# Kernel tuning notes

Hardware: AMD Instinct MI355X
Metric: run time of the kernel (lower is better)

Reference implementation:

```python
import jax, jax.numpy as jnp
import numpy as np

B, L, D_MODEL = 2, 2048, 1024
D_INNER, D_STATE, D_CONV, DT_RANK = 2048, 16, 4, 64  # expand=2, dt_rank=ceil(1024/16)


def setup_inputs() -> dict:
    key = jax.random.key(0)
    ks = jax.random.split(key, 12)
    s = lambda k, shape, sc=0.02: jax.random.normal(k, shape, dtype=jnp.float32) * sc
    return {
        "x": jax.random.normal(ks[0], (B, L, D_MODEL), dtype=jnp.float32),
        "norm_w": jnp.ones((D_MODEL,), jnp.float32),
        "norm_b": jnp.zeros((D_MODEL,), jnp.float32),
        "in_proj_w": s(ks[1], (2 * D_INNER, D_MODEL)),
        "conv_w": s(ks[2], (D_INNER, 1, D_CONV), 0.1),
        "conv_b": s(ks[3], (D_INNER,), 0.1),
        "x_proj_w": s(ks[4], (DT_RANK + 2 * D_STATE, D_INNER)),
        "dt_proj_w": s(ks[5], (D_INNER, DT_RANK), 0.1),
        "dt_proj_b": s(ks[6], (D_INNER,), 0.5),
        "A_log": jnp.log(jnp.broadcast_to(jnp.arange(1, D_STATE + 1, dtype=jnp.float32), (D_INNER, D_STATE))),
        "D": jnp.ones((D_INNER,), jnp.float32),
        "out_proj_w": s(ks[7], (D_MODEL, D_INNER)),
    }


def _layernorm(x, w, b, eps=1e-5):
    mu = jnp.mean(x, axis=-1, keepdims=True)
    var = jnp.var(x, axis=-1, keepdims=True)
    return (x - mu) * jax.lax.rsqrt(var + eps) * w + b


def _mamba_forward(x, norm_w, norm_b, in_proj_w, conv_w, conv_b, x_proj_w,
                   dt_proj_w, dt_proj_b, A_log, D, out_proj_w):
    residual = x
    xn = _layernorm(x, norm_w, norm_b)
    # in_proj -> split into x-branch and gate z
    xz = jnp.einsum('bld,ed->ble', xn, in_proj_w)  # [B,L,2*D_INNER]
    xc, z = jnp.split(xz, 2, axis=-1)
    # causal depthwise conv1d over time
    xt = jnp.transpose(xc, (0, 2, 1))  # [B,C,L]
    xt = jnp.pad(xt, ((0, 0), (0, 0), (D_CONV - 1, 0)))
    xt = jax.lax.conv_general_dilated(
        xt, conv_w, window_strides=(1,), padding=[(0, 0)],
        feature_group_count=D_INNER,
        dimension_numbers=('NCH', 'OIH', 'NCH')) + conv_b[None, :, None]
    u = jax.nn.silu(jnp.transpose(xt, (0, 2, 1)))  # [B,L,D_INNER]
    # input-dependent dt, B, C
    x_dbl = jnp.einsum('bld,ed->ble', u, x_proj_w)
    dt, Bm, Cm = jnp.split(x_dbl, [DT_RANK, DT_RANK + D_STATE], axis=-1)
    dt = jax.nn.softplus(jnp.einsum('blr,dr->bld', dt, dt_proj_w) + dt_proj_b)  # [B,L,D_INNER]
    A = -jnp.exp(A_log)  # [D_INNER, D_STATE]

    def step(h, inp):
        dt_t, B_t, C_t, u_t = inp  # [B,Di],[B,Ds],[B,Ds],[B,Di]
        dA = jnp.exp(dt_t[..., None] * A)                       # [B,Di,Ds]
        h = dA * h + (dt_t * u_t)[..., None] * B_t[:, None, :]  # [B,Di,Ds]
        y_t = jnp.einsum('bds,bs->bd', h, C_t)
        return h, y_t

    xs = (jnp.transpose(dt, (1, 0, 2)), jnp.transpose(Bm, (1, 0, 2)),
          jnp.transpose(Cm, (1, 0, 2)), jnp.transpose(u, (1, 0, 2)))
    h0 = jnp.zeros((B, D_INNER, D_STATE), dtype=x.dtype)
    _, ys = jax.lax.scan(step, h0, xs)
    y = jnp.transpose(ys, (1, 0, 2)) + u * D  # [B,L,D_INNER]
    y = y * jax.nn.silu(z)
    out = jnp.einsum('ble,de->bld', y, out_proj_w)
    # dropout in eval mode = identity
    return residual + out


def reference(x, norm_w, norm_b, in_proj_w, conv_w, conv_b, x_proj_w,
              dt_proj_w, dt_proj_b, A_log, D, out_proj_w):
    return _mamba_forward(x, norm_w, norm_b, in_proj_w, conv_w, conv_b, x_proj_w,
                          dt_proj_w, dt_proj_b, A_log, D, out_proj_w)
```

## Files before the change

### kernel.cpp

```cpp
#include <hip/hip_runtime.h>
#include <hip/hip_bf16.h>
#include <math.h>

#define BB 2
#define LL 2048
#define DMODEL 1024
#define DINNER 2048
#define DSTATE 16
#define DTRANK 64
#define NROWS (BB * LL)
#define NC 64
#define CK 32
#define KS 16
#define KCH (DINNER / KS)

typedef __bf16 bf16x8 __attribute__((ext_vector_type(8)));
typedef float  f32x4  __attribute__((ext_vector_type(4)));
typedef ushort us8    __attribute__((ext_vector_type(8)));
typedef __attribute__((address_space(3))) void       as3_void;
typedef const __attribute__((address_space(1))) void as1_cvoid;

__device__ __forceinline__ ushort f2bf(float x) {
    __hip_bfloat16 h = __float2bfloat16(x);
    return *(ushort*)&h;
}
__device__ __forceinline__ float bf2f(ushort u) {
    unsigned int v = ((unsigned int)u) << 16;
    return *(float*)&v;
}

__global__ __launch_bounds__(256) void ln_kernel(const float* __restrict__ x,
                                                 const float* __restrict__ w,
                                                 const float* __restrict__ b,
                                                 __hip_bfloat16* __restrict__ xn) {
    int row = blockIdx.x;
    const float* xr = x + (size_t)row * DMODEL;
    float4 v = reinterpret_cast<const float4*>(xr)[threadIdx.x];
    float s  = v.x + v.y + v.z + v.w;
    float ss = v.x * v.x + v.y * v.y + v.z * v.z + v.w * v.w;
    for (int off = 32; off > 0; off >>= 1) {
        s  += __shfl_down(s, off);
        ss += __shfl_down(ss, off);
    }
    __shared__ float red0[4], red1[4];
    __shared__ float mu_s, rstd_s;
    int lane = threadIdx.x & 63, wv = threadIdx.x >> 6;
    if (lane == 0) { red0[wv] = s; red1[wv] = ss; }
    __syncthreads();
    if (threadIdx.x == 0) {
        float S = red0[0] + red0[1] + red0[2] + red0[3];
        float SS = red1[0] + red1[1] + red1[2] + red1[3];
        float mu = S * (1.0f / DMODEL);
        float var = SS * (1.0f / DMODEL) - mu * mu;
        mu_s = mu;
        rstd_s = rsqrtf(var + 1e-5f);
    }
    __syncthreads();
    float mu = mu_s, rstd = rstd_s;
    float4 wv4 = reinterpret_cast<const float4*>(w)[threadIdx.x];
    float4 bv4 = reinterpret_cast<const float4*>(b)[threadIdx.x];
    ushort4 o;
    o.x = f2bf((v.x - mu) * rstd * wv4.x + bv4.x);
    o.y = f2bf((v.y - mu) * rstd * wv4.y + bv4.y);
    o.z = f2bf((v.z - mu) * rstd * wv4.z + bv4.z);
    o.w = f2bf((v.w - mu) * rstd * wv4.w + bv4.w);
    *reinterpret_cast<ushort4*>((ushort*)xn + (size_t)row * DMODEL + threadIdx.x * 4) = o;
}

__global__ __launch_bounds__(256) void cvt_kernel(const float* __restrict__ in,
                                                  __hip_bfloat16* __restrict__ o) {
    int i = (blockIdx.x * 256 + threadIdx.x) * 4;
    float4 v = *reinterpret_cast<const float4*>(in + i);
    ushort4 p;
    p.x = f2bf(v.x); p.y = f2bf(v.y); p.z = f2bf(v.z); p.w = f2bf(v.w);
    *reinterpret_cast<ushort4*>((ushort*)o + i) = p;
}

template <int EPI>
__global__ __launch_bounds__(256) void gemm_bf16(
    const __hip_bfloat16* __restrict__ A, int lda,
    const __hip_bfloat16* __restrict__ W, int ldw,
    void* __restrict__ C, void* __restrict__ C2, int nsplit, int ldc,
    int K, const float* __restrict__ R) {
    __shared__ ushort As[128][32];
    __shared__ ushort Bs[128][32];
    int tid = threadIdx.x;
    int w = tid >> 6, lane = tid & 63;
    int m0 = blockIdx.y * 128, n0 = blockIdx.x * 128;
    int wr = w >> 1, wc = w & 1;

    int srow = (w << 4) + (lane >> 2);
    int skoff = (lane & 3) << 3;
    const ushort* gA = (const ushort*)A + (size_t)(m0 + srow) * lda + skoff;
    const ushort* gB = (const ushort*)W + (size_t)(n0 + srow) * ldw + skoff;
    char* ldsA0 = (char*)&As[0][0] + w * 1024;
    char* ldsB0 = (char*)&Bs[0][0] + w * 1024;

    f32x4 acc[4][4] = {};
    int frow = (lane & 15);
    int fk   = (lane >> 4) << 3;

    for (int k0 = 0; k0 < K; k0 += 32) {
        __syncthreads();
        __builtin_amdgcn_global_load_lds((as1_cvoid*)(gA + k0),                    (as3_void*)(ldsA0),        16, 0, 0);
        __builtin_amdgcn_global_load_lds((as1_cvoid*)(gA + (size_t)64 * lda + k0), (as3_void*)(ldsA0 + 4096), 16, 0, 0);
        __builtin_amdgcn_global_load_lds((as1_cvoid*)(gB + k0),                    (as3_void*)(ldsB0),        16, 0, 0);
        __builtin_amdgcn_global_load_lds((as1_cvoid*)(gB + (size_t)64 * ldw + k0), (as3_void*)(ldsB0 + 4096), 16, 0, 0);
        __syncthreads();

        bf16x8 af[4], bfr[4];
#pragma unroll
        for (int mi = 0; mi < 4; mi++)
            af[mi] = *(const bf16x8*)&As[wr * 64 + mi * 16 + frow][fk];
#pragma unroll
        for (int ni = 0; ni < 4; ni++)
            bfr[ni] = *(const bf16x8*)&Bs[wc * 64 + ni * 16 + frow][fk];
#pragma unroll
        for (int mi = 0; mi < 4; mi++)
#pragma unroll
            for (int ni = 0; ni < 4; ni++)
                acc[mi][ni] = __builtin_amdgcn_mfma_f32_16x16x32_bf16(
                    af[mi], bfr[ni], acc[mi][ni], 0, 0, 0);
    }

    int crow = (lane >> 4) << 2;
    int ccol = lane & 15;
    bool toz = (EPI == 0) && (n0 >= nsplit);
    int nbase = toz ? (n0 - nsplit) : n0;
    ushort* Cu = toz ? (ushort*)C2 : (ushort*)C;
#pragma unroll
    for (int mi = 0; mi < 4; mi++) {
#pragma unroll
        for (int ni = 0; ni < 4; ni++) {
#pragma unroll
            for (int r = 0; r < 4; r++) {
                int m = m0 + wr * 64 + mi * 16 + crow + r;
                int n = nbase + wc * 64 + ni * 16 + ccol;
                float v = acc[mi][ni][r];
                if (EPI == 2) {
                    v += R[(size_t)m * ldc + n];
                    ((float*)C)[(size_t)m * ldc + n] = v;
                } else if (EPI == 1) {
                    v += R[n];
                    v = (v > 20.f) ? v : log1pf(__expf(v));
                    ((ushort*)C)[(size_t)m * ldc + n] = f2bf(v);
                } else {
                    Cu[(size_t)m * ldc + n] = f2bf(v);
                }
            }
        }
    }
}

__global__ __launch_bounds__(256) void xp_partial(
    const ushort* __restrict__ A,
    const float* __restrict__ W,
    float* __restrict__ P) {
    __shared__ float As[16][64];
    __shared__ float Ws[16][64];
    int m0 = blockIdx.y * 64;
    int n0 = blockIdx.x * 64;
    int kbase = blockIdx.z * KCH;
    int tid = threadIdx.x;
    int tm = tid >> 4, tn = tid & 15;
    int lr = tid >> 2;
    int lk = (tid & 3) << 2;

    float acc[4][4] = {};

    for (int k0 = kbase; k0 < kbase + KCH; k0 += 16) {
        ushort4 au = *reinterpret_cast<const ushort4*>(A + (size_t)(m0 + lr) * DINNER + k0 + lk);
        float4 av = make_float4(bf2f(au.x), bf2f(au.y), bf2f(au.z), bf2f(au.w));
        float4 wvv;
        int wn = n0 + lr;
        if (wn < 96)
            wvv = *reinterpret_cast<const float4*>(W + (size_t)wn * DINNER + k0 + lk);
        else
            wvv = make_float4(0.f, 0.f, 0.f, 0.f);
        __syncthreads();
        As[lk + 0][lr] = av.x; As[lk + 1][lr] = av.y;
        As[lk + 2][lr] = av.z; As[lk + 3][lr] = av.w;
        Ws[lk + 0][lr] = wvv.x; Ws[lk + 1][lr] = wvv.y;
        Ws[lk + 2][lr] = wvv.z; Ws[lk + 3][lr] = wvv.w;
        __syncthreads();
#pragma unroll
        for (int k = 0; k < 16; k++) {
            float4 a = *reinterpret_cast<const float4*>(&As[k][tm << 2]);
            float4 bv = *reinterpret_cast<const float4*>(&Ws[k][tn << 2]);
            float ar[4] = {a.x, a.y, a.z, a.w};
            float br[4] = {bv.x, bv.y, bv.z, bv.w};
#pragma unroll
            for (int i = 0; i < 4; i++)
#pragma unroll
                for (int j = 0; j < 4; j++)
                    acc[i][j] = fmaf(ar[i], br[j], acc[i][j]);
        }
    }
    float* Pz = P + (size_t)blockIdx.z * NROWS * 96;
#pragma unroll
    for (int i = 0; i < 4; i++) {
        int m = m0 + (tm << 2) + i;
#pragma unroll
        for (int j = 0; j < 4; j++) {
            int n = n0 + (tn << 2) + j;
            if (n < 96)
                Pz[(size_t)m * 96 + n] = acc[i][j];
        }
    }
}

__global__ __launch_bounds__(256) void xp_reduce(
    const float* __restrict__ P, float* __restrict__ xdbl,
    ushort* __restrict__ xdbl16) {
    int i = blockIdx.x * 256 + threadIdx.x;
    float s = 0.f;
#pragma unroll
    for (int z = 0; z < KS; z++)
        s += P[(size_t)z * NROWS * 96 + i];
    xdbl[i] = s;
    xdbl16[i] = f2bf(s);
}

__global__ __launch_bounds__(256) void conv_silu_kernel(
    const ushort* __restrict__ xc16, const float* __restrict__ cw,
    const float* __restrict__ cb, ushort* __restrict__ u16) {
    int r = blockIdx.x;
    int l = r & (LL - 1);
    int c0 = threadIdx.x << 3;
    const ushort* base = xc16 + (size_t)r * DINNER + c0;
    us8 z8 = {0, 0, 0, 0, 0, 0, 0, 0};
    us8 v0 = *(const us8*)(base);
    us8 v1 = (l >= 1) ? *(const us8*)(base - DINNER)     : z8;
    us8 v2 = (l >= 2) ? *(const us8*)(base - 2 * DINNER) : z8;
    us8 v3 = (l >= 3) ? *(const us8*)(base - 3 * DINNER) : z8;
    us8 o;
#pragma unroll
    for (int j = 0; j < 8; j++) {
        float4 wj = reinterpret_cast<const float4*>(cw)[c0 + j];
        float acc = cb[c0 + j];
        acc = fmaf(bf2f(v3[j]), wj.x, acc);
        acc = fmaf(bf2f(v2[j]), wj.y, acc);
        acc = fmaf(bf2f(v1[j]), wj.z, acc);
        acc = fmaf(bf2f(v0[j]), wj.w, acc);
        float sig = 1.f / (1.f + __expf(-acc));
        o[j] = f2bf(acc * sig);
    }
    *(us8*)(u16 + (size_t)r * DINNER + c0) = o;
}

__global__ __launch_bounds__(256) void scan_pass1(
    const ushort* __restrict__ dt16, const ushort* __restrict__ u16,
    const float* __restrict__ xdbl, const float* __restrict__ A_log,
    float* __restrict__ hloc, float* __restrict__ aprod) {
    int bc = blockIdx.x >> 3;
    int b = bc >> 6, c = bc & (NC - 1);
    int d = ((blockIdx.x & 7) << 8) + threadIdx.x;
    float a2[DSTATE];
#pragma unroll
    for (int s = 0; s < DSTATE; s++)
        a2[s] = -__expf(A_log[d * DSTATE + s]) * 1.44269504089f;
    float h[DSTATE], ap[DSTATE];
#pragma unroll
    for (int s = 0; s < DSTATE; s++) { h[s] = 0.f; ap[s] = 1.f; }

    int t0 = c * CK;
    const ushort* dtp = dt16 + ((size_t)b * LL + t0) * DINNER + d;
    const ushort* up  = u16  + ((size_t)b * LL + t0) * DINNER + d;
    const float* xr0  = xdbl + ((size_t)b * LL + t0) * 96;

    for (int t = 0; t < CK; t++) {
        float dtv = bf2f(dtp[(size_t)t * DINNER]);
        float uv  = bf2f(up[(size_t)t * DINNER]);
        float du  = dtv * uv;
        const float* xr = xr0 + t * 96;
#pragma unroll
        for (int s = 0; s < DSTATE; s++) {
            float dA = exp2f(dtv * a2[s]);
            h[s] = fmaf(dA, h[s], du * xr[64 + s]);
            ap[s] *= dA;
        }
    }
    size_t base = ((size_t)bc * DSTATE) * DINNER + d;
#pragma unroll
    for (int s = 0; s < DSTATE; s++) {
        hloc[base + (size_t)s * DINNER]  = h[s];
        aprod[base + (size_t)s * DINNER] = ap[s];
    }
}

__global__ __launch_bounds__(256) void scan_pass2(
    float* __restrict__ hloc, const float* __restrict__ aprod) {
    int idx = blockIdx.x * 256 + threadIdx.x;
    int d = idx & (DINNER - 1);
    int s = (idx >> 11) & (DSTATE - 1);
    int b = idx >> 15;
    float run = 0.f;
    for (int c = 0; c < NC; c++) {
        size_t off = ((size_t)((b * NC + c) * DSTATE + s)) * DINNER + d;
        float hl = hloc[off];
        float ap = aprod[off];
        hloc[off] = run;
        run = fmaf(ap, run, hl);
    }
}

__global__ __launch_bounds__(256) void scan_pass3(
    const ushort* __restrict__ dt16, const ushort* __restrict__ u16,
    const float* __restrict__ xdbl, const ushort* __restrict__ zb,
    const float* __restrict__ A_log, const float* __restrict__ Dp,
    const float* __restrict__ hinit, __hip_bfloat16* __restrict__ y) {
    int bc = blockIdx.x >> 3;
    int b = bc >> 6, c = bc & (NC - 1);
    int d = ((blockIdx.x & 7) << 8) + threadIdx.x;
    float a2[DSTATE];
#pragma unroll
    for (int s = 0; s < DSTATE; s++)
        a2[s] = -__expf(A_log[d * DSTATE + s]) * 1.44269504089f;
    float Dd = Dp[d];
    float h[DSTATE];
    size_t base = ((size_t)bc * DSTATE) * DINNER + d;
#pragma unroll
    for (int s = 0; s < DSTATE; s++) h[s] = hinit[base + (size_t)s * DINNER];

    int t0 = c * CK;
    const ushort* dtp = dt16 + ((size_t)b * LL + t0) * DINNER + d;
    const ushort* up  = u16  + ((size_t)b * LL + t0) * DINNER + d;
    const ushort* zp  = zb   + ((size_t)b * LL + t0) * DINNER + d;
    const float* xr0  = xdbl + ((size_t)b * LL + t0) * 96;
    ushort* yp = (ushort*)y + ((size_t)b * LL + t0) * DINNER + d;

    for (int t = 0; t < CK; t++) {
        float dtv = bf2f(dtp[(size_t)t * DINNER]);
        float uv  = bf2f(up[(size_t)t * DINNER]);
        float du  = dtv * uv;
        const float* xr = xr0 + t * 96;
        float yv = 0.f;
#pragma unroll
        for (int s = 0; s < DSTATE; s++) {
            float dA = exp2f(dtv * a2[s]);
            h[s] = fmaf(dA, h[s], du * xr[64 + s]);
            yv = fmaf(h[s], xr[80 + s], yv);
        }
        float zv = bf2f(zp[(size_t)t * DINNER]);
        float sig = 1.f / (1.f + __expf(-zv));
        yv = (yv + uv * Dd) * (zv * sig);
        yp[(size_t)t * DINNER] = f2bf(yv);
    }
}

extern "C" void kernel_launch(void* const* d_in, const int* in_sizes, int n_in,
                              void* d_out, int out_size, void* d_ws, size_t ws_size,
                              hipStream_t stream) {
    const float* x         = (const float*)d_in[0];
    const float* norm_w    = (const float*)d_in[1];
    const float* norm_b    = (const float*)d_in[2];
    const float* in_proj_w = (const float*)d_in[3];
    const float* conv_w    = (const float*)d_in[4];
    const float* conv_b    = (const float*)d_in[5];
    const float* x_proj_w  = (const float*)d_in[6];
    const float* dt_proj_w = (const float*)d_in[7];
    const float* dt_proj_b = (const float*)d_in[8];
    const float* A_log     = (const float*)d_in[9];
    const float* Dp        = (const float*)d_in[10];
    const float* out_proj_w= (const float*)d_in[11];
    float* out = (float*)d_out;

    float* ws   = (float*)d_ws;
    const size_t NI = (size_t)NROWS * DINNER;
    ushort* xc16  = (ushort*)ws;
    ushort* zb    = (ushort*)(ws + NI / 2);
    ushort* u16   = (ushort*)(ws + NI);
    ushort* dt16  = (ushort*)(ws + NI + NI / 2);
    float*  xdbl  = ws + 2 * NI;
    ushort* xdbl16 = (ushort*)(xdbl + (size_t)NROWS * 96);
    float*  nxt   = xdbl + (size_t)NROWS * 96 + (size_t)NROWS * 96 / 2;
    __hip_bfloat16* xnb = (__hip_bfloat16*)nxt;
    __hip_bfloat16* ybb = xnb + (size_t)NROWS * DMODEL;
    __hip_bfloat16* wib = ybb + NI;
    __hip_bfloat16* wob = wib + (size_t)2 * DINNER * DMODEL;
    __hip_bfloat16* wdt = wob + (size_t)DMODEL * DINNER;
    float* hloc  = (float*)(wdt + (size_t)DINNER * DTRANK);
    float* aprod = hloc + NI / 2;
    float* xpp   = aprod + NI / 2;

    ln_kernel<<<NROWS, 256, 0, stream>>>(x, norm_w, norm_b, xnb);
    cvt_kernel<<<(2 * DINNER * DMODEL) / 1024, 256, 0, stream>>>(in_proj_w, wib);
    cvt_kernel<<<(DMODEL * DINNER) / 1024, 256, 0, stream>>>(out_proj_w, wob);
    cvt_kernel<<<(DINNER * DTRANK) / 1024, 256, 0, stream>>>(dt_proj_w, wdt);
    gemm_bf16<0><<<dim3((2 * DINNER) / 128, NROWS / 128), 256, 0, stream>>>(
        xnb, DMODEL, wib, DMODEL, xc16, zb, DINNER, DINNER, DMODEL, nullptr);
    conv_silu_kernel<<<NROWS, 256, 0, stream>>>(xc16, conv_w, conv_b, u16);
    xp_partial<<<dim3(2, NROWS / 64, KS), 256, 0, stream>>>(u16, x_proj_w, xpp);
    xp_reduce<<<(NROWS * 96) / 256, 256, 0, stream>>>(xpp, xdbl, xdbl16);
    gemm_bf16<1><<<dim3(DINNER / 128, NROWS / 128), 256, 0, stream>>>(
        (const __hip_bfloat16*)xdbl16, 96, wdt, DTRANK,
        dt16, nullptr, 1 << 30, DINNER, DTRANK, dt_proj_b);
    scan_pass1<<<BB * NC * (DINNER / 256), 256, 0, stream>>>(
        dt16, u16, xdbl, A_log, hloc, aprod);
    scan_pass2<<<(BB * DSTATE * DINNER) / 256, 256, 0, stream>>>(hloc, aprod);
    scan_pass3<<<BB * NC * (DINNER / 256), 256, 0, stream>>>(
        dt16, u16, xdbl, zb, A_log, Dp, hloc, ybb);
    gemm_bf16<2><<<dim3(DMODEL / 128, NROWS / 128), 256, 0, stream>>>(
        ybb, DINNER, wob, DINNER, out, nullptr, 1 << 30, DMODEL, DINNER, x);
}
```

Baseline: 411.0 us.

## Move x_proj GEMM to bf16 MFMA and halve scan chunk length

Replaces the fp32 SIMT split-K x_proj kernel with a bf16 MFMA kernel that stages tiles through direct global-to-LDS loads, using a weight copy converted and zero-padded to 128 rows. The scan chunk count doubles (chunk length halves), raising parallelism in passes 1 and 3 at the cost of a longer serial pass 2 and larger hloc/aprod buffers. The workspace is also rearranged so the split-K partials alias hloc and y aliases aprod. The x_proj weights now run in bf16 instead of fp32, lowering precision, and the padded weight adds a little wasted compute.

After: 442.2 us. 1.08x slower.

```diff
diff --git a/kernel.cpp b/kernel.cpp
--- a/kernel.cpp
+++ b/kernel.cpp
@@ -9,8 +9,8 @@
 #define DSTATE 16
 #define DTRANK 64
 #define NROWS (BB * LL)
-#define NC 64
-#define CK 32
+#define NC 128
+#define CK 16
 #define KS 16
 #define KCH (DINNER / KS)
 
@@ -74,6 +74,14 @@
     ushort4 p;
     p.x = f2bf(v.x); p.y = f2bf(v.y); p.z = f2bf(v.z); p.w = f2bf(v.w);
     *reinterpret_cast<ushort4*>((ushort*)o + i) = p;
+}
+
+__global__ __launch_bounds__(256) void cvtpad_kernel(const float* __restrict__ in,
+                                                     __hip_bfloat16* __restrict__ o) {
+    int i = blockIdx.x * 256 + threadIdx.x;
+    int n = i >> 11, k = i & (DINNER - 1);
+    float v = (n < 96) ? in[n * DINNER + k] : 0.f;
+    ((ushort*)o)[i] = f2bf(v);
 }
 
 template <int EPI>
@@ -152,59 +160,67 @@
     }
 }
 
-__global__ __launch_bounds__(256) void xp_partial(
+__global__ __launch_bounds__(256) void xp_mfma(
     const ushort* __restrict__ A,
-    const float* __restrict__ W,
+    const __hip_bfloat16* __restrict__ W,
     float* __restrict__ P) {
-    __shared__ float As[16][64];
-    __shared__ float Ws[16][64];
-    int m0 = blockIdx.y * 64;
-    int n0 = blockIdx.x * 64;
-    int kbase = blockIdx.z * KCH;
+    __shared__ ushort As[128][32];
+    __shared__ ushort Bs[128][32];
     int tid = threadIdx.x;
-    int tm = tid >> 4, tn = tid & 15;
-    int lr = tid >> 2;
-    int lk = (tid & 3) << 2;
-
-    float acc[4][4] = {};
-
-    for (int k0 = kbase; k0 < kbase + KCH; k0 += 16) {
-        ushort4 au = *reinterpret_cast<const ushort4*>(A + (size_t)(m0 + lr) * DINNER + k0 + lk);
-        float4 av = make_float4(bf2f(au.x), bf2f(au.y), bf2f(au.z), bf2f(au.w));
-        float4 wvv;
-        int wn = n0 + lr;
-        if (wn < 96)
-            wvv = *reinterpret_cast<const float4*>(W + (size_t)wn * DINNER + k0 + lk);
-        else
-            wvv = make_float4(0.f, 0.f, 0.f, 0.f);
+    int w = tid >> 6, lane = tid & 63;
+    int m0 = blockIdx.y * 128;
+    int kz = blockIdx.z;
+    int wr = w >> 1, wc = w & 1;
+
+    int srow = (w << 4) + (lane >> 2);
+    int skoff = (lane & 3) << 3;
+    const ushort* gA = A + (size_t)(m0 + srow) * DINNER + skoff;
+    const ushort* gB = (const ushort*)W + (size_t)srow * DINNER + skoff;
+    char* ldsA0 = (char*)&As[0][0] + w * 1024;
+    char* ldsB0 = (char*)&Bs[0][0] + w * 1024;
+
+    f32x4 acc[4][4] = {};
+    int frow = (lane & 15);
+    int fk   = (lane >> 4) << 3;
+    int kbeg = kz * KCH;
+
+    for (int k0 = kbeg; k0 < kbeg + KCH; k0 += 32) {
         __syncthreads();
-        As[lk + 0][lr] = av.x; As[lk + 1][lr] = av.y;
-        As[lk + 2][lr] = av.z; As[lk + 3][lr] = av.w;
-        Ws[lk + 0][lr] = wvv.x; Ws[lk + 1][lr] = wvv.y;
-        Ws[lk + 2][lr] = wvv.z; Ws[lk + 3][lr] = wvv.w;
+        __builtin_amdgcn_global_load_lds((as1_cvoid*)(gA + k0),                       (as3_void*)(ldsA0),        16, 0, 0);
+        __builtin_amdgcn_global_load_lds((as1_cvoid*)(gA + (size_t)64 * DINNER + k0), (as3_void*)(ldsA0 + 4096), 16, 0, 0);
+        __builtin_amdgcn_global_load_lds((as1_cvoid*)(gB + k0),                       (as3_void*)(ldsB0),        16, 0, 0);
+        __builtin_amdgcn_global_load_lds((as1_cvoid*)(gB + (size_t)64 * DINNER + k0), (as3_void*)(ldsB0 + 4096), 16, 0, 0);
         __syncthreads();
-#pragma unroll
-        for (int k = 0; k < 16; k++) {
-            float4 a = *reinterpret_cast<const float4*>(&As[k][tm << 2]);
-            float4 bv = *reinterpret_cast<const float4*>(&Ws[k][tn << 2]);
-            float ar[4] = {a.x, a.y, a.z, a.w};
-            float br[4] = {bv.x, bv.y, bv.z, bv.w};
-#pragma unroll
-            for (int i = 0; i < 4; i++)
-#pragma unroll
-                for (int j = 0; j < 4; j++)
-                    acc[i][j] = fmaf(ar[i], br[j], acc[i][j]);
-        }
-    }
-    float* Pz = P + (size_t)blockIdx.z * NROWS * 96;
-#pragma unroll
-    for (int i = 0; i < 4; i++) {
-        int m = m0 + (tm << 2) + i;
-#pragma unroll
-        for (int j = 0; j < 4; j++) {
-            int n = n0 + (tn << 2) + j;
-            if (n < 96)
-                Pz[(size_t)m * 96 + n] = acc[i][j];
+
+        bf16x8 af[4], bfr[4];
+#pragma unroll
+        for (int mi = 0; mi < 4; mi++)
+            af[mi] = *(const bf16x8*)&As[wr * 64 + mi * 16 + frow][fk];
+#pragma unroll
+        for (int ni = 0; ni < 4; ni++)
+            bfr[ni] = *(const bf16x8*)&Bs[wc * 64 + ni * 16 + frow][fk];
+#pragma unroll
+        for (int mi = 0; mi < 4; mi++)
+#pragma unroll
+            for (int ni = 0; ni < 4; ni++)
+                acc[mi][ni] = __builtin_amdgcn_mfma_f32_16x16x32_bf16(
+                    af[mi], bfr[ni], acc[mi][ni], 0, 0, 0);
+    }
+
+    int crow = (lane >> 4) << 2;
+    int ccol = lane & 15;
+    float* Pz = P + (size_t)kz * NROWS * 96;
+#pragma unroll
+    for (int mi = 0; mi < 4; mi++) {
+#pragma unroll
+        for (int ni = 0; ni < 4; ni++) {
+#pragma unroll
+            for (int r = 0; r < 4; r++) {
+                int m = m0 + wr * 64 + mi * 16 + crow + r;
+                int n = wc * 64 + ni * 16 + ccol;
+                if (n < 96)
+                    Pz[(size_t)m * 96 + n] = acc[mi][ni][r];
+            }
         }
     }
 }
@@ -253,7 +269,7 @@
     const float* __restrict__ xdbl, const float* __restrict__ A_log,
     float* __restrict__ hloc, float* __restrict__ aprod) {
     int bc = blockIdx.x >> 3;
-    int b = bc >> 6, c = bc & (NC - 1);
+    int b = bc >> 7, c = bc & (NC - 1);
     int d = ((blockIdx.x & 7) << 8) + threadIdx.x;
     float a2[DSTATE];
 #pragma unroll
@@ -310,7 +326,7 @@
     const float* __restrict__ A_log, const float* __restrict__ Dp,
     const float* __restrict__ hinit, __hip_bfloat16* __restrict__ y) {
     int bc = blockIdx.x >> 3;
-    int b = bc >> 6, c = bc & (NC - 1);
+    int b = bc >> 7, c = bc & (NC - 1);
     int d = ((blockIdx.x & 7) << 8) + threadIdx.x;
     float a2[DSTATE];
 #pragma unroll
@@ -375,22 +391,24 @@
     ushort* xdbl16 = (ushort*)(xdbl + (size_t)NROWS * 96);
     float*  nxt   = xdbl + (size_t)NROWS * 96 + (size_t)NROWS * 96 / 2;
     __hip_bfloat16* xnb = (__hip_bfloat16*)nxt;
-    __hip_bfloat16* ybb = xnb + (size_t)NROWS * DMODEL;
-    __hip_bfloat16* wib = ybb + NI;
+    __hip_bfloat16* wib = xnb + (size_t)NROWS * DMODEL;
     __hip_bfloat16* wob = wib + (size_t)2 * DINNER * DMODEL;
     __hip_bfloat16* wdt = wob + (size_t)DMODEL * DINNER;
-    float* hloc  = (float*)(wdt + (size_t)DINNER * DTRANK);
-    float* aprod = hloc + NI / 2;
-    float* xpp   = aprod + NI / 2;
+    __hip_bfloat16* wxp = wdt + (size_t)DINNER * DTRANK;
+    float* hloc  = (float*)(wxp + (size_t)128 * DINNER);
+    float* aprod = hloc + (size_t)BB * NC * DSTATE * DINNER;
+    float* xpp = hloc;
+    __hip_bfloat16* ybb = (__hip_bfloat16*)aprod;
 
     ln_kernel<<<NROWS, 256, 0, stream>>>(x, norm_w, norm_b, xnb);
     cvt_kernel<<<(2 * DINNER * DMODEL) / 1024, 256, 0, stream>>>(in_proj_w, wib);
     cvt_kernel<<<(DMODEL * DINNER) / 1024, 256, 0, stream>>>(out_proj_w, wob);
     cvt_kernel<<<(DINNER * DTRANK) / 1024, 256, 0, stream>>>(dt_proj_w, wdt);
+    cvtpad_kernel<<<(128 * DINNER) / 256, 256, 0, stream>>>(x_proj_w, wxp);
     gemm_bf16<0><<<dim3((2 * DINNER) / 128, NROWS / 128), 256, 0, stream>>>(
         xnb, DMODEL, wib, DMODEL, xc16, zb, DINNER, DINNER, DMODEL, nullptr);
     conv_silu_kernel<<<NROWS, 256, 0, stream>>>(xc16, conv_w, conv_b, u16);
-    xp_partial<<<dim3(2, NROWS / 64, KS), 256, 0, stream>>>(u16, x_proj_w, xpp);
+    xp_mfma<<<dim3(1, NROWS / 128, KS), 256, 0, stream>>>(u16, wxp, xpp);
     xp_reduce<<<(NROWS * 96) / 256, 256, 0, stream>>>(xpp, xdbl, xdbl16);
     gemm_bf16<1><<<dim3(DINNER / 128, NROWS / 128), 256, 0, stream>>>(
         (const __hip_bfloat16*)xdbl16, 96, wdt, DTRANK,
```
